# Optimization experiments

Hardware: AMD Instinct MI355X
Metric: run time of the kernel (lower is better)

The kernel has to match this reference:

```python
import jax, jax.numpy as jnp
import numpy as np

B, C, H, W = 8, 384, 32, 32
HEADS, DIM_HEAD = 6, 64
INNER = HEADS * DIM_HEAD  # 384


def setup_inputs() -> dict:
    key = jax.random.key(0)
    ks = jax.random.split(key, 6)
    s = 0.02
    return {
        "query": jax.random.normal(ks[0], (B, C, H, W), jnp.float32),
        "context": jax.random.normal(ks[1], (B, C, H, W), jnp.float32),
        "Wq": jax.random.normal(ks[2], (INNER, C), jnp.float32) * s,
        "Wk": jax.random.normal(ks[3], (INNER, C), jnp.float32) * s,
        "Wv": jax.random.normal(ks[4], (INNER, C), jnp.float32) * s,
        "Wo": jax.random.normal(ks[5], (C, INNER), jnp.float32) * s,
        "bo": jnp.zeros((C,), jnp.float32),
    }


def reference(query, context, Wq, Wk, Wv, Wo, bo):
    scale = DIM_HEAD ** (-0.5)
    b, _, h, w = query.shape
    n = h * w  # tokens
    # 1x1 convs == channel-wise linear projections
    q = jnp.einsum('bchw,oc->bohw', query, Wq)
    k = jnp.einsum('bchw,oc->bohw', context, Wk)
    v = jnp.einsum('bchw,oc->bohw', context, Wv)
    # split heads: [B, heads, dim_head, N]
    q = q.reshape(b, HEADS, DIM_HEAD, n)
    k = k.reshape(b, HEADS, DIM_HEAD, n)
    v = v.reshape(b, HEADS, DIM_HEAD, n)
    # attn[b,h,i,j] = sum_d q[b,h,d,i] k[b,h,d,j] * scale
    attn = jax.nn.softmax(jnp.einsum('bhdn,bhdm->bhnm', q, k) * scale, axis=-1)
    # out[b,h,i,d] = sum_j attn[b,h,i,j] v[b,h,d,j]
    out = jnp.einsum('bhnm,bhdm->bhdn', attn, v)  # [B, heads, dim_head, N]
    out = out.reshape(b, INNER, h, w)
    out = jnp.einsum('bchw,oc->bohw', out, Wo) + bo[None, :, None, None]
    attn_map = attn.mean(axis=(1, 2)).reshape(b, h, w)
    return out, attn_map
```

## Files before the change

kernel.cpp:

```cpp
#include <hip/hip_runtime.h>

#define BATCH 8
#define CCH   384
#define NTOK  1024
#define HEADS 6
#define DHEAD 64
#define QSCALE 0.18033688011112042f

typedef __bf16 bf16x8 __attribute__((ext_vector_type(8)));
typedef float  f32x4  __attribute__((ext_vector_type(4)));

#define MFMA16(a, b, c) __builtin_amdgcn_mfma_f32_16x16x32_bf16((a), (b), (c), 0, 0, 0)

__device__ __forceinline__ short f2b(float x) {
    unsigned u = __float_as_uint(x);
    u += 0x7fffu + ((u >> 16) & 1u);
    return (short)(u >> 16);
}

__device__ __forceinline__ void gld_lds16(const short* gp, short* lp) {
    __builtin_amdgcn_global_load_lds(
        (const __attribute__((address_space(1))) void*)gp,
        (__attribute__((address_space(3))) void*)lp, 16, 0, 0);
}

__device__ __forceinline__ void stage_tile(const short* gbase, size_t gstride,
                                           short* lbase, int wv, int lane) {
#pragma unroll
    for (int t = 0; t < 2; ++t) {
        const int row = t * 8 + (lane >> 3);
        const int c   = (lane & 7) ^ (row & 7);
        gld_lds16(gbase + (size_t)(wv * 16 + row) * gstride + c * 8,
                  lbase + (wv * 16 + t * 8) * 64);
    }
}
__device__ __forceinline__ bf16x8 frag_read(const short* lbase, int row, int c) {
    const int pc = c ^ (row & 7);
    return *(const bf16x8*)(lbase + row * 64 + pc * 8);
}

__device__ __forceinline__ void gemm128_core(
    const short* __restrict__ Ag, const short* __restrict__ Bg,
    short* Ast, short* Bst, f32x4 acc[4][4])
{
    const int tid = threadIdx.x, lane = tid & 63;
    const int l15 = tid & 15, quad = (tid >> 4) & 3, wv = tid >> 6;

    stage_tile(Ag, CCH, Ast, wv, lane);
    stage_tile(Ag + 64 * CCH, CCH, Ast + 4096, wv, lane);
    stage_tile(Bg, CCH, Bst, wv, lane);
    stage_tile(Bg + 64 * CCH, CCH, Bst + 4096, wv, lane);
    __syncthreads();

#pragma unroll
    for (int kc = 0; kc < 6; ++kc) {
        const int cur = kc & 1;
        if (kc < 5) {
            short* An = Ast + (cur ^ 1) * 8192;
            short* Bn = Bst + (cur ^ 1) * 8192;
            stage_tile(Ag + (kc + 1) * 64, CCH, An, wv, lane);
            stage_tile(Ag + (kc + 1) * 64 + 64 * CCH, CCH, An + 4096, wv, lane);
            stage_tile(Bg + (kc + 1) * 64, CCH, Bn, wv, lane);
            stage_tile(Bg + (kc + 1) * 64 + 64 * CCH, CCH, Bn + 4096, wv, lane);
        }
        const short* Atile = Ast + cur * 8192 + (wv >> 1) * 4096;
        const short* Btile = Bst + cur * 8192 + (wv & 1) * 4096;
#pragma unroll
        for (int h = 0; h < 2; ++h) {
            bf16x8 a[4], b[4];
#pragma unroll
            for (int s = 0; s < 4; ++s) {
                a[s] = frag_read(Atile, s * 16 + l15, h * 4 + quad);
                b[s] = frag_read(Btile, s * 16 + l15, h * 4 + quad);
            }
#pragma unroll
            for (int si = 0; si < 4; ++si)
#pragma unroll
                for (int sj = 0; sj < 4; ++sj)
                    acc[si][sj] = MFMA16(a[si], b[sj], acc[si][sj]);
        }
        __syncthreads();
    }
}

__device__ __forceinline__ void epilogue_bf16(
    f32x4 acc[4][4], short* cbuf,
    short* __restrict__ out, size_t obase, int ostride)
{
    const int tid = threadIdx.x;
    const int l15 = tid & 15, quad = (tid >> 4) & 3, wv = tid >> 6;
    const int wi = (wv >> 1) * 64, wj = (wv & 1) * 64;
    __syncthreads();
#pragma unroll
    for (int si = 0; si < 4; ++si)
#pragma unroll
        for (int sj = 0; sj < 4; ++sj)
#pragma unroll
            for (int rr = 0; rr < 4; ++rr)
                cbuf[(wi + si * 16 + quad * 4 + rr) * 128 + wj + sj * 16 + l15] =
                    f2b(acc[si][sj][rr]);
    __syncthreads();
#pragma unroll
    for (int pass = 0; pass < 8; ++pass) {
        const int row = pass * 16 + (tid >> 4);
        bf16x8 vchunk = *(const bf16x8*)(cbuf + row * 128 + l15 * 8);
        *(bf16x8*)(out + obase + (size_t)row * ostride + l15 * 8) = vchunk;
    }
}

__global__ __launch_bounds__(256) void prep(
    const float* __restrict__ Xq, const float* __restrict__ Xc,
    const float* __restrict__ w0, const float* __restrict__ w1,
    const float* __restrict__ w2, const float* __restrict__ w3,
    short* __restrict__ Xtq, short* __restrict__ Xtc,
    short* __restrict__ o0, short* __restrict__ o1,
    short* __restrict__ o2, short* __restrict__ o3,
    float* __restrict__ amap)
{
    __shared__ float tile[64][65];
    const int id = blockIdx.x, tid = threadIdx.x;
    if (id < 1536) {
        const int zz = id % 16, t = id / 16;
        const int n0 = (t % 16) * 64, c0 = (t / 16) * 64;
        const float* X = (zz < 8) ? Xq : Xc;
        short* Xt      = (zz < 8) ? Xtq : Xtc;
        const int b = zz & 7;
        const int tx = tid & 15, ty = tid >> 4;
#pragma unroll
        for (int rr = 0; rr < 4; ++rr) {
            const int c = rr * 16 + ty;
            float4 v = *(const float4*)&X[((size_t)(b * CCH + c0 + c)) * NTOK + n0 + tx * 4];
            tile[c][tx * 4 + 0] = v.x; tile[c][tx * 4 + 1] = v.y;
            tile[c][tx * 4 + 2] = v.z; tile[c][tx * 4 + 3] = v.w;
        }
        __syncthreads();
        const int n = tid >> 2, cb = (tid & 3) * 16;
        short tmp[16];
#pragma unroll
        for (int cc = 0; cc < 16; ++cc) tmp[cc] = f2b(tile[cb + cc][n]);
        short* dst = &Xt[((size_t)(b * NTOK + n0 + n)) * CCH + c0 + cb];
        *(int4*)dst = *(int4*)&tmp[0];
        *(int4*)(dst + 8) = *(int4*)&tmp[8];
    } else if (id < 2112) {
        const int w = id - 1536;
        const int which = w / 144;
        const int idx = (w % 144) * 256 + tid;
        const float* s = which == 0 ? w0 : which == 1 ? w1 : which == 2 ? w2 : w3;
        short* d       = which == 0 ? o0 : which == 1 ? o1 : which == 2 ? o2 : o3;
        float4 v = ((const float4*)s)[idx];
        short4 o = make_short4(f2b(v.x), f2b(v.y), f2b(v.z), f2b(v.w));
        ((short4*)d)[idx] = o;
    } else {
        const int o = (id - 2112) * 1024 + tid * 4;
        float4 z = {0.f, 0.f, 0.f, 0.f};
        *(float4*)&amap[o] = z;
    }
}

__global__ __launch_bounds__(256, 2) void gemm_qkv(
    const short* __restrict__ xtq, const short* __restrict__ xtc,
    const short* __restrict__ wq, const short* __restrict__ wk,
    const short* __restrict__ wvm,
    short* __restrict__ qout, short* __restrict__ kout, short* __restrict__ vout)
{
    __shared__ __align__(16) short Ast[2][8192];
    __shared__ __align__(16) short Bst[2][8192];
    const int id = blockIdx.x;
    const int b = id & 7, r = id >> 3;
    const int which = r / 24, tt = r % 24;

    const short *Ag, *Bg;
    short* out;
    size_t obase;
    int ostride;
    if (which < 2) {
        const int it = tt / 3, jt = tt % 3;
        const short* x = (which == 0) ? xtq : xtc;
        const short* W = (which == 0) ? wq : wk;
        Ag = x + ((size_t)(b * NTOK + it * 128)) * CCH;
        Bg = W + (size_t)(jt * 128) * CCH;
        out = (which == 0) ? qout : kout;
        obase = ((size_t)(b * NTOK + it * 128)) * CCH + jt * 128;
        ostride = CCH;
    } else {
        const int ct = tt % 3, nt = tt / 3;
        Ag = wvm + (size_t)(ct * 128) * CCH;
        Bg = xtc + ((size_t)(b * NTOK + nt * 128)) * CCH;
        out = vout;
        obase = ((size_t)(b * CCH + ct * 128)) * NTOK + nt * 128;
        ostride = NTOK;
    }

    f32x4 z4 = {0.f, 0.f, 0.f, 0.f};
    f32x4 acc[4][4];
#pragma unroll
    for (int si = 0; si < 4; ++si)
#pragma unroll
        for (int sj = 0; sj < 4; ++sj) acc[si][sj] = z4;

    gemm128_core(Ag, Bg, &Ast[0][0], &Bst[0][0], acc);

    if (which == 0) {
#pragma unroll
        for (int si = 0; si < 4; ++si)
#pragma unroll
            for (int sj = 0; sj < 4; ++sj)
#pragma unroll
                for (int rr = 0; rr < 4; ++rr)
                    acc[si][sj][rr] *= QSCALE;
    }
    epilogue_bf16(acc, &Ast[0][0], out, obase, ostride);
}

__global__ __launch_bounds__(256, 2) void o_proj(
    const short* __restrict__ wo, const short* __restrict__ omid,
    const float* __restrict__ bias, float* __restrict__ Y)
{
    __shared__ __align__(16) short Ast[2][8192];
    __shared__ __align__(16) short Bst[2][8192];
    const int id = blockIdx.x;
    const int b = id & 7, r = id >> 3;
    const int ct = r % 3, nt = r / 3;

    const short* Ag = wo + (size_t)(ct * 128) * CCH;
    const short* Bg = omid + ((size_t)(b * NTOK + nt * 128)) * CCH;

    f32x4 z4 = {0.f, 0.f, 0.f, 0.f};
    f32x4 acc[4][4];
#pragma unroll
    for (int si = 0; si < 4; ++si)
#pragma unroll
        for (int sj = 0; sj < 4; ++sj) acc[si][sj] = z4;

    gemm128_core(Ag, Bg, &Ast[0][0], &Bst[0][0], acc);

    const int tid = threadIdx.x;
    const int l15 = tid & 15, quad = (tid >> 4) & 3, wv = tid >> 6;
    const int wi = (wv >> 1) * 64, wj = (wv & 1) * 64;
#pragma unroll
    for (int si = 0; si < 4; ++si) {
#pragma unroll
        for (int rr = 0; rr < 4; ++rr) {
            const int ch = ct * 128 + wi + si * 16 + quad * 4 + rr;
            const float bv = bias[ch];
#pragma unroll
            for (int sj = 0; sj < 4; ++sj)
                Y[((size_t)(b * CCH + ch)) * NTOK + nt * 128 + wj + sj * 16 + l15] =
                    acc[si][sj][rr] + bv;
        }
    }
}

__global__ __launch_bounds__(256) void attn(
    const short* __restrict__ qt, const short* __restrict__ kt,
    const short* __restrict__ vc, short* __restrict__ omid,
    float* __restrict__ amap)
{
    __shared__ __align__(16) short Kst[2][64 * 64];
    __shared__ __align__(16) short Vst[2][64 * 64];
    __shared__ __align__(16) short Pst[4][16][64];
    __shared__ float colbuf[2][4][64];

    const int tid = threadIdx.x, lane = tid & 63;
    const int l15 = tid & 15, quad = (tid >> 4) & 3, wv = tid >> 6;
    const int id = blockIdx.x;
    const int b = id & 7, rr_ = id >> 3;
    const int h = rr_ % 6, i0 = (rr_ / 6) * 64;

    const size_t hoff = (size_t)b * NTOK * CCH + h * DHEAD;
    const short* Kg = kt + hoff;
    const short* Vg = vc + ((size_t)(b * CCH + h * DHEAD)) * NTOK;

    const short* qp = qt + hoff + (size_t)(i0 + wv * 16 + l15) * CCH + quad * 8;
    const bf16x8 qa0 = *(const bf16x8*)qp;
    const bf16x8 qa1 = *(const bf16x8*)(qp + 32);

    stage_tile(Kg, CCH, Kst[0], wv, lane);
    __syncthreads();

    float den[4] = {0.f, 0.f, 0.f, 0.f};
    for (int jt = 0; jt < 16; ++jt) {
        const int cur = jt & 1;
        if (jt < 15)
            stage_tile(Kg + (size_t)(jt + 1) * 64 * CCH, CCH, Kst[cur ^ 1], wv, lane);
        f32x4 z4 = {0.f, 0.f, 0.f, 0.f};
        f32x4 s[4] = {z4, z4, z4, z4};
#pragma unroll
        for (int ns = 0; ns < 4; ++ns) {
            const int row = ns * 16 + l15;
            bf16x8 k0 = frag_read(Kst[cur], row, quad);
            bf16x8 k1 = frag_read(Kst[cur], row, quad + 4);
            s[ns] = MFMA16(qa0, k0, s[ns]);
            s[ns] = MFMA16(qa1, k1, s[ns]);
        }
#pragma unroll
        for (int ns = 0; ns < 4; ++ns)
#pragma unroll
            for (int r = 0; r < 4; ++r)
                den[r] += exp2f(s[ns][r]);
        __syncthreads();
    }
#pragma unroll
    for (int r = 0; r < 4; ++r) {
        den[r] += __shfl_xor(den[r], 1);
        den[r] += __shfl_xor(den[r], 2);
        den[r] += __shfl_xor(den[r], 4);
        den[r] += __shfl_xor(den[r], 8);
    }
    float rden[4];
#pragma unroll
    for (int r = 0; r < 4; ++r) rden[r] = 1.0f / den[r];

    stage_tile(Kg, CCH, Kst[0], wv, lane);
    stage_tile(Vg, NTOK, Vst[0], wv, lane);
    __syncthreads();

    f32x4 z4o = {0.f, 0.f, 0.f, 0.f};
    f32x4 oacc[4] = {z4o, z4o, z4o, z4o};
    for (int jt = 0; jt < 16; ++jt) {
        const int cur = jt & 1;
        if (jt < 15) {
            stage_tile(Kg + (size_t)(jt + 1) * 64 * CCH, CCH, Kst[cur ^ 1], wv, lane);
            stage_tile(Vg + (size_t)(jt + 1) * 64, NTOK, Vst[cur ^ 1], wv, lane);
        }
        f32x4 s[4] = {z4o, z4o, z4o, z4o};
#pragma unroll
        for (int ns = 0; ns < 4; ++ns) {
            const int row = ns * 16 + l15;
            bf16x8 k0 = frag_read(Kst[cur], row, quad);
            bf16x8 k1 = frag_read(Kst[cur], row, quad + 4);
            s[ns] = MFMA16(qa0, k0, s[ns]);
            s[ns] = MFMA16(qa1, k1, s[ns]);
        }
        float p[4][4];
#pragma unroll
        for (int ns = 0; ns < 4; ++ns)
#pragma unroll
            for (int r = 0; r < 4; ++r)
                p[ns][r] = exp2f(s[ns][r]) * rden[r];

#pragma unroll
        for (int ns = 0; ns < 4; ++ns) {
            float cs = p[ns][0] + p[ns][1] + p[ns][2] + p[ns][3];
            cs += __shfl_xor(cs, 16);
            cs += __shfl_xor(cs, 32);
            if (quad == 0) colbuf[cur][wv][ns * 16 + l15] = cs;
        }

#pragma unroll
        for (int ns = 0; ns < 4; ++ns) {
            const int c = ns * 2 + (l15 >> 3);
#pragma unroll
            for (int r = 0; r < 4; ++r) {
                const int row = quad * 4 + r;
                Pst[wv][row][((c ^ (row & 7)) << 3) | (l15 & 7)] = f2b(p[ns][r]);
            }
        }
        asm volatile("" ::: "memory");
        const int pc0 = quad ^ (l15 & 7);
        const int pc1 = (quad + 4) ^ (l15 & 7);
        bf16x8 pa0 = *(const bf16x8*)&Pst[wv][l15][pc0 * 8];
        bf16x8 pa1 = *(const bf16x8*)&Pst[wv][l15][pc1 * 8];
        asm volatile("" ::: "memory");

#pragma unroll
        for (int ds = 0; ds < 4; ++ds) {
            const int row = ds * 16 + l15;
            bf16x8 v0 = frag_read(Vst[cur], row, quad);
            bf16x8 v1 = frag_read(Vst[cur], row, quad + 4);
            oacc[ds] = MFMA16(pa0, v0, oacc[ds]);
            oacc[ds] = MFMA16(pa1, v1, oacc[ds]);
        }
        __syncthreads();
        if (tid < 64) {
            const float t = colbuf[cur][0][tid] + colbuf[cur][1][tid]
                          + colbuf[cur][2][tid] + colbuf[cur][3][tid];
            atomicAdd(amap + (size_t)b * NTOK + jt * 64 + tid,
                      t * (1.0f / (HEADS * NTOK)));
        }
    }

#pragma unroll
    for (int ds = 0; ds < 4; ++ds)
#pragma unroll
        for (int r = 0; r < 4; ++r) {
            const int i = i0 + wv * 16 + quad * 4 + r;
            omid[((size_t)(b * NTOK + i)) * CCH + h * DHEAD + ds * 16 + l15] =
                f2b(oacc[ds][r]);
        }
}

extern "C" void kernel_launch(void* const* d_in, const int* in_sizes, int n_in,
                              void* d_out, int out_size, void* d_ws, size_t ws_size,
                              hipStream_t stream)
{
    const float* query   = (const float*)d_in[0];
    const float* context = (const float*)d_in[1];
    const float* Wq      = (const float*)d_in[2];
    const float* Wk      = (const float*)d_in[3];
    const float* Wv      = (const float*)d_in[4];
    const float* Wo      = (const float*)d_in[5];
    const float* bo      = (const float*)d_in[6];

    float* out = (float*)d_out;
    const size_t out_elems = (size_t)BATCH * CCH * NTOK;
    float* attn_map = out + out_elems;

    short* ws = (short*)d_ws;
    const size_t XT = (size_t)BATCH * NTOK * CCH;
    const size_t WSZ = (size_t)CCH * CCH;
    short* xtq  = ws;
    short* xtc  = xtq + XT;
    short* wqb  = xtc + XT;
    short* wkb  = wqb + WSZ;
    short* wvb  = wkb + WSZ;
    short* wob  = wvb + WSZ;
    short* qtb  = wob + WSZ;
    short* ktb  = qtb + XT;
    short* vcb  = ktb + XT;
    short* omid = vcb + XT;

    const dim3 blk(256);

    prep<<<dim3(2120), blk, 0, stream>>>(query, context, Wq, Wk, Wv, Wo,
                                         xtq, xtc, wqb, wkb, wvb, wob, attn_map);

    gemm_qkv<<<dim3(576), blk, 0, stream>>>(xtq, xtc, wqb, wkb, wvb,
                                            qtb, ktb, vcb);

    attn<<<dim3(768), blk, 0, stream>>>(qtb, ktb, vcb, omid, attn_map);

    o_proj<<<dim3(192), blk, 0, stream>>>(wob, omid, bo, out);
}
```

Baseline: 167.3 us.

## Fuse four kernels into persistent megakernel with software grid barriers

Measured after the change: 449.8 us. +168.9%, slower.

```diff
diff --git a/kernel.cpp b/kernel.cpp
--- a/kernel.cpp
+++ b/kernel.cpp
@@ -7,6 +7,8 @@
 #define DHEAD 64
 #define QSCALE 0.18033688011112042f
 
+#define NBLK 512
+
 typedef __bf16 bf16x8 __attribute__((ext_vector_type(8)));
 typedef float  f32x4  __attribute__((ext_vector_type(4)));
 
@@ -39,32 +41,34 @@
     return *(const bf16x8*)(lbase + row * 64 + pc * 8);
 }
 
-__device__ __forceinline__ void gemm128_core(
+__device__ __forceinline__ void gbar(int* cnt) {
+    __syncthreads();
+    if (threadIdx.x == 0) {
+        __threadfence();
+        __hip_atomic_fetch_add(cnt, 1, __ATOMIC_RELEASE, __HIP_MEMORY_SCOPE_AGENT);
+        while (__hip_atomic_load(cnt, __ATOMIC_ACQUIRE, __HIP_MEMORY_SCOPE_AGENT) < NBLK)
+            __builtin_amdgcn_s_sleep(2);
+        __threadfence();
+    }
+    __syncthreads();
+}
+
+__device__ __forceinline__ void gemm128_core_sb(
     const short* __restrict__ Ag, const short* __restrict__ Bg,
     short* Ast, short* Bst, f32x4 acc[4][4])
 {
     const int tid = threadIdx.x, lane = tid & 63;
     const int l15 = tid & 15, quad = (tid >> 4) & 3, wv = tid >> 6;
 
-    stage_tile(Ag, CCH, Ast, wv, lane);
-    stage_tile(Ag + 64 * CCH, CCH, Ast + 4096, wv, lane);
-    stage_tile(Bg, CCH, Bst, wv, lane);
-    stage_tile(Bg + 64 * CCH, CCH, Bst + 4096, wv, lane);
-    __syncthreads();
-
 #pragma unroll
     for (int kc = 0; kc < 6; ++kc) {
-        const int cur = kc & 1;
-        if (kc < 5) {
-            short* An = Ast + (cur ^ 1) * 8192;
-            short* Bn = Bst + (cur ^ 1) * 8192;
-            stage_tile(Ag + (kc + 1) * 64, CCH, An, wv, lane);
-            stage_tile(Ag + (kc + 1) * 64 + 64 * CCH, CCH, An + 4096, wv, lane);
-            stage_tile(Bg + (kc + 1) * 64, CCH, Bn, wv, lane);
-            stage_tile(Bg + (kc + 1) * 64 + 64 * CCH, CCH, Bn + 4096, wv, lane);
-        }
-        const short* Atile = Ast + cur * 8192 + (wv >> 1) * 4096;
-        const short* Btile = Bst + cur * 8192 + (wv & 1) * 4096;
+        stage_tile(Ag + kc * 64, CCH, Ast, wv, lane);
+        stage_tile(Ag + kc * 64 + 64 * CCH, CCH, Ast + 4096, wv, lane);
+        stage_tile(Bg + kc * 64, CCH, Bst, wv, lane);
+        stage_tile(Bg + kc * 64 + 64 * CCH, CCH, Bst + 4096, wv, lane);
+        __syncthreads();
+        const short* Atile = Ast + (wv >> 1) * 4096;
+        const short* Btile = Bst + (wv & 1) * 4096;
 #pragma unroll
         for (int h = 0; h < 2; ++h) {
             bf16x8 a[4], b[4];
@@ -108,18 +112,16 @@
     }
 }
 
-__global__ __launch_bounds__(256) void prep(
-    const float* __restrict__ Xq, const float* __restrict__ Xc,
-    const float* __restrict__ w0, const float* __restrict__ w1,
-    const float* __restrict__ w2, const float* __restrict__ w3,
-    short* __restrict__ Xtq, short* __restrict__ Xtc,
-    short* __restrict__ o0, short* __restrict__ o1,
-    short* __restrict__ o2, short* __restrict__ o3,
-    float* __restrict__ amap)
-{
-    __shared__ float tile[64][65];
-    const int id = blockIdx.x, tid = threadIdx.x;
+__device__ __forceinline__ void prep_unit(
+    int id, char* smem,
+    const float* Xq, const float* Xc,
+    const float* w0, const float* w1, const float* w2, const float* w3,
+    short* Xtq, short* Xtc,
+    short* o0, short* o1, short* o2, short* o3, float* amap)
+{
+    const int tid = threadIdx.x;
     if (id < 1536) {
+        float (*tile)[65] = (float(*)[65])smem;
         const int zz = id % 16, t = id / 16;
         const int n0 = (t % 16) * 64, c0 = (t / 16) * 64;
         const float* X = (zz < 8) ? Xq : Xc;
@@ -157,15 +159,14 @@
     }
 }
 
-__global__ __launch_bounds__(256, 2) void gemm_qkv(
-    const short* __restrict__ xtq, const short* __restrict__ xtc,
-    const short* __restrict__ wq, const short* __restrict__ wk,
-    const short* __restrict__ wvm,
-    short* __restrict__ qout, short* __restrict__ kout, short* __restrict__ vout)
-{
-    __shared__ __align__(16) short Ast[2][8192];
-    __shared__ __align__(16) short Bst[2][8192];
-    const int id = blockIdx.x;
+__device__ __forceinline__ void gemm_qkv_unit(
+    int id, char* smem,
+    const short* xtq, const short* xtc,
+    const short* wq, const short* wk, const short* wvm,
+    short* qout, short* kout, short* vout)
+{
+    short* Ast = (short*)smem;
+    short* Bst = (short*)(smem + 16384);
     const int b = id & 7, r = id >> 3;
     const int which = r / 24, tt = r % 24;
 
@@ -198,7 +199,7 @@
 #pragma unroll
         for (int sj = 0; sj < 4; ++sj) acc[si][sj] = z4;
 
-    gemm128_core(Ag, Bg, &Ast[0][0], &Bst[0][0], acc);
+    gemm128_core_sb(Ag, Bg, Ast, Bst, acc);
 
     if (which == 0) {
 #pragma unroll
@@ -209,16 +210,15 @@
                 for (int rr = 0; rr < 4; ++rr)
                     acc[si][sj][rr] *= QSCALE;
     }
-    epilogue_bf16(acc, &Ast[0][0], out, obase, ostride);
-}
-
-__global__ __launch_bounds__(256, 2) void o_proj(
-    const short* __restrict__ wo, const short* __restrict__ omid,
-    const float* __restrict__ bias, float* __restrict__ Y)
-{
-    __shared__ __align__(16) short Ast[2][8192];
-    __shared__ __align__(16) short Bst[2][8192];
-    const int id = blockIdx.x;
+    epilogue_bf16(acc, (short*)smem, out, obase, ostride);
+}
+
+__device__ __forceinline__ void o_proj_unit(
+    int id, char* smem,
+    const short* wo, const short* omid, const float* bias, float* Y)
+{
+    short* Ast = (short*)smem;
+    short* Bst = (short*)(smem + 16384);
     const int b = id & 7, r = id >> 3;
     const int ct = r % 3, nt = r / 3;
 
@@ -232,7 +232,7 @@
 #pragma unroll
         for (int sj = 0; sj < 4; ++sj) acc[si][sj] = z4;
 
-    gemm128_core(Ag, Bg, &Ast[0][0], &Bst[0][0], acc);
+    gemm128_core_sb(Ag, Bg, Ast, Bst, acc);
 
     const int tid = threadIdx.x;
     const int l15 = tid & 15, quad = (tid >> 4) & 3, wv = tid >> 6;
@@ -251,19 +251,18 @@
     }
 }
 
-__global__ __launch_bounds__(256) void attn(
-    const short* __restrict__ qt, const short* __restrict__ kt,
-    const short* __restrict__ vc, short* __restrict__ omid,
-    float* __restrict__ amap)
-{
-    __shared__ __align__(16) short Kst[2][64 * 64];
-    __shared__ __align__(16) short Vst[2][64 * 64];
-    __shared__ __align__(16) short Pst[4][16][64];
-    __shared__ float colbuf[2][4][64];
+__device__ __forceinline__ void attn_unit(
+    int id, char* smem,
+    const short* qt, const short* kt, const short* vc,
+    short* omid, float* amap)
+{
+    short* Kst    = (short*)smem;
+    short* Vst    = (short*)(smem + 16384);
+    short* Pst    = (short*)(smem + 32768);
+    float* colbuf = (float*)(smem + 40960);
 
     const int tid = threadIdx.x, lane = tid & 63;
     const int l15 = tid & 15, quad = (tid >> 4) & 3, wv = tid >> 6;
-    const int id = blockIdx.x;
     const int b = id & 7, rr_ = id >> 3;
     const int h = rr_ % 6, i0 = (rr_ / 6) * 64;
 
@@ -275,21 +274,22 @@
     const bf16x8 qa0 = *(const bf16x8*)qp;
     const bf16x8 qa1 = *(const bf16x8*)(qp + 32);
 
-    stage_tile(Kg, CCH, Kst[0], wv, lane);
+    stage_tile(Kg, CCH, Kst, wv, lane);
     __syncthreads();
 
     float den[4] = {0.f, 0.f, 0.f, 0.f};
     for (int jt = 0; jt < 16; ++jt) {
         const int cur = jt & 1;
         if (jt < 15)
-            stage_tile(Kg + (size_t)(jt + 1) * 64 * CCH, CCH, Kst[cur ^ 1], wv, lane);
+            stage_tile(Kg + (size_t)(jt + 1) * 64 * CCH, CCH,
+                       Kst + (cur ^ 1) * 4096, wv, lane);
         f32x4 z4 = {0.f, 0.f, 0.f, 0.f};
         f32x4 s[4] = {z4, z4, z4, z4};
 #pragma unroll
         for (int ns = 0; ns < 4; ++ns) {
             const int row = ns * 16 + l15;
-            bf16x8 k0 = frag_read(Kst[cur], row, quad);
-            bf16x8 k1 = frag_read(Kst[cur], row, quad + 4);
+            bf16x8 k0 = frag_read(Kst + cur * 4096, row, quad);
+            bf16x8 k1 = frag_read(Kst + cur * 4096, row, quad + 4);
             s[ns] = MFMA16(qa0, k0, s[ns]);
             s[ns] = MFMA16(qa1, k1, s[ns]);
         }
@@ -311,8 +311,8 @@
 #pragma unroll
     for (int r = 0; r < 4; ++r) rden[r] = 1.0f / den[r];
 
-    stage_tile(Kg, CCH, Kst[0], wv, lane);
-    stage_tile(Vg, NTOK, Vst[0], wv, lane);
+    stage_tile(Kg, CCH, Kst, wv, lane);
+    stage_tile(Vg, NTOK, Vst, wv, lane);
     __syncthreads();
 
     f32x4 z4o = {0.f, 0.f, 0.f, 0.f};
@@ -320,15 +320,17 @@
     for (int jt = 0; jt < 16; ++jt) {
         const int cur = jt & 1;
         if (jt < 15) {
-            stage_tile(Kg + (size_t)(jt + 1) * 64 * CCH, CCH, Kst[cur ^ 1], wv, lane);
-            stage_tile(Vg + (size_t)(jt + 1) * 64, NTOK, Vst[cur ^ 1], wv, lane);
+            stage_tile(Kg + (size_t)(jt + 1) * 64 * CCH, CCH,
+                       Kst + (cur ^ 1) * 4096, wv, lane);
+            stage_tile(Vg + (size_t)(jt + 1) * 64, NTOK,
+                       Vst + (cur ^ 1) * 4096, wv, lane);
         }
         f32x4 s[4] = {z4o, z4o, z4o, z4o};
 #pragma unroll
         for (int ns = 0; ns < 4; ++ns) {
             const int row = ns * 16 + l15;
-            bf16x8 k0 = frag_read(Kst[cur], row, quad);
-            bf16x8 k1 = frag_read(Kst[cur], row, quad + 4);
+            bf16x8 k0 = frag_read(Kst + cur * 4096, row, quad);
+            bf16x8 k1 = frag_read(Kst + cur * 4096, row, quad + 4);
             s[ns] = MFMA16(qa0, k0, s[ns]);
             s[ns] = MFMA16(qa1, k1, s[ns]);
         }
@@ -344,7 +346,7 @@
             float cs = p[ns][0] + p[ns][1] + p[ns][2] + p[ns][3];
             cs += __shfl_xor(cs, 16);
             cs += __shfl_xor(cs, 32);
-            if (quad == 0) colbuf[cur][wv][ns * 16 + l15] = cs;
+            if (quad == 0) colbuf[cur * 256 + wv * 64 + ns * 16 + l15] = cs;
         }
 
 #pragma unroll
@@ -353,28 +355,31 @@
 #pragma unroll
             for (int r = 0; r < 4; ++r) {
                 const int row = quad * 4 + r;
-                Pst[wv][row][((c ^ (row & 7)) << 3) | (l15 & 7)] = f2b(p[ns][r]);
+                Pst[wv * 1024 + row * 64 + (((c ^ (row & 7)) << 3) | (l15 & 7))] =
+                    f2b(p[ns][r]);
             }
         }
         asm volatile("" ::: "memory");
         const int pc0 = quad ^ (l15 & 7);
         const int pc1 = (quad + 4) ^ (l15 & 7);
-        bf16x8 pa0 = *(const bf16x8*)&Pst[wv][l15][pc0 * 8];
-        bf16x8 pa1 = *(const bf16x8*)&Pst[wv][l15][pc1 * 8];
+        bf16x8 pa0 = *(const bf16x8*)&Pst[wv * 1024 + l15 * 64 + pc0 * 8];
+        bf16x8 pa1 = *(const bf16x8*)&Pst[wv * 1024 + l15 * 64 + pc1 * 8];
         asm volatile("" ::: "memory");
 
 #pragma unroll
         for (int ds = 0; ds < 4; ++ds) {
             const int row = ds * 16 + l15;
-            bf16x8 v0 = frag_read(Vst[cur], row, quad);
-            bf16x8 v1 = frag_read(Vst[cur], row, quad + 4);
+            bf16x8 v0 = frag_read(Vst + cur * 4096, row, quad);
+            bf16x8 v1 = frag_read(Vst + cur * 4096, row, quad + 4);
             oacc[ds] = MFMA16(pa0, v0, oacc[ds]);
             oacc[ds] = MFMA16(pa1, v1, oacc[ds]);
         }
         __syncthreads();
         if (tid < 64) {
-            const float t = colbuf[cur][0][tid] + colbuf[cur][1][tid]
-                          + colbuf[cur][2][tid] + colbuf[cur][3][tid];
+            const float t = colbuf[cur * 256 + 0 * 64 + tid]
+                          + colbuf[cur * 256 + 1 * 64 + tid]
+                          + colbuf[cur * 256 + 2 * 64 + tid]
+                          + colbuf[cur * 256 + 3 * 64 + tid];
             atomicAdd(amap + (size_t)b * NTOK + jt * 64 + tid,
                       t * (1.0f / (HEADS * NTOK)));
         }
@@ -388,6 +393,42 @@
             omid[((size_t)(b * NTOK + i)) * CCH + h * DHEAD + ds * 16 + l15] =
                 f2b(oacc[ds][r]);
         }
+}
+
+__global__ __launch_bounds__(256, 2) void mega(
+    const float* __restrict__ Xq, const float* __restrict__ Xc,
+    const float* __restrict__ w0, const float* __restrict__ w1,
+    const float* __restrict__ w2, const float* __restrict__ w3,
+    const float* __restrict__ bo,
+    short* xtq, short* xtc,
+    short* wqb, short* wkb, short* wvb, short* wob,
+    short* qtb, short* ktb, short* vcb, short* omid,
+    float* out, float* amap, int* bar)
+{
+    __shared__ __align__(16) char smem[43008];
+    const int bid = blockIdx.x;
+
+    for (int u = bid; u < 2120; u += NBLK) {
+        prep_unit(u, smem, Xq, Xc, w0, w1, w2, w3,
+                  xtq, xtc, wqb, wkb, wvb, wob, amap);
+        __syncthreads();
+    }
+    gbar(&bar[0]);
+
+    for (int u = bid; u < 576; u += NBLK) {
+        gemm_qkv_unit(u, smem, xtq, xtc, wqb, wkb, wvb, qtb, ktb, vcb);
+        __syncthreads();
+    }
+    gbar(&bar[1]);
+
+    for (int u = bid; u < 768; u += NBLK) {
+        attn_unit(u, smem, qtb, ktb, vcb, omid, amap);
+        __syncthreads();
+    }
+    gbar(&bar[2]);
+
+    if (bid < 192)
+        o_proj_unit(bid, smem, wob, omid, bo, out);
 }
 
 extern "C" void kernel_launch(void* const* d_in, const int* in_sizes, int n_in,
@@ -419,16 +460,12 @@
     short* ktb  = qtb + XT;
     short* vcb  = ktb + XT;
     short* omid = vcb + XT;
-
-    const dim3 blk(256);
-
-    prep<<<dim3(2120), blk, 0, stream>>>(query, context, Wq, Wk, Wv, Wo,
-                                         xtq, xtc, wqb, wkb, wvb, wob, attn_map);
-
-    gemm_qkv<<<dim3(576), blk, 0, stream>>>(xtq, xtc, wqb, wkb, wvb,
-                                            qtb, ktb, vcb);
-
-    attn<<<dim3(768), blk, 0, stream>>>(qtb, ktb, vcb, omid, attn_map);
-
-    o_proj<<<dim3(192), blk, 0, stream>>>(wob, omid, bo, out);
-}
+    int*   bar  = (int*)(omid + XT);
+
+    hipMemsetAsync(bar, 0, 4 * sizeof(int), stream);
+
+    mega<<<dim3(NBLK), dim3(256), 0, stream>>>(
+        query, context, Wq, Wk, Wv, Wo, bo,
+        xtq, xtc, wqb, wkb, wvb, wob,
+        qtb, ktb, vcb, omid, out, attn_map, bar);
+}
```

## Double attention query tile per block to share K/V staging across eight waves

Applied to the files above, without the earlier changes.

New measurement: 169.3 us. No clear change (+1.2%).

```diff
diff --git a/kernel.cpp b/kernel.cpp
--- a/kernel.cpp
+++ b/kernel.cpp
@@ -33,6 +33,13 @@
         gld_lds16(gbase + (size_t)(wv * 16 + row) * gstride + c * 8,
                   lbase + (wv * 16 + t * 8) * 64);
     }
+}
+__device__ __forceinline__ void stage_tile8(const short* gbase, size_t gstride,
+                                            short* lbase, int wv, int lane) {
+    const int row = wv * 8 + (lane >> 3);
+    const int c   = (lane & 7) ^ (row & 7);
+    gld_lds16(gbase + (size_t)row * gstride + c * 8,
+              lbase + (wv * 8) * 64);
 }
 __device__ __forceinline__ bf16x8 frag_read(const short* lbase, int row, int c) {
     const int pc = c ^ (row & 7);
@@ -251,21 +258,21 @@
     }
 }
 
-__global__ __launch_bounds__(256) void attn(
+__global__ __launch_bounds__(512) void attn(
     const short* __restrict__ qt, const short* __restrict__ kt,
     const short* __restrict__ vc, short* __restrict__ omid,
     float* __restrict__ amap)
 {
     __shared__ __align__(16) short Kst[2][64 * 64];
     __shared__ __align__(16) short Vst[2][64 * 64];
-    __shared__ __align__(16) short Pst[4][16][64];
-    __shared__ float colbuf[2][4][64];
+    __shared__ __align__(16) short Pst[8][16][64];
+    __shared__ float colbuf[2][8][64];
 
     const int tid = threadIdx.x, lane = tid & 63;
     const int l15 = tid & 15, quad = (tid >> 4) & 3, wv = tid >> 6;
     const int id = blockIdx.x;
     const int b = id & 7, rr_ = id >> 3;
-    const int h = rr_ % 6, i0 = (rr_ / 6) * 64;
+    const int h = rr_ % 6, i0 = (rr_ / 6) * 128;
 
     const size_t hoff = (size_t)b * NTOK * CCH + h * DHEAD;
     const short* Kg = kt + hoff;
@@ -275,14 +282,14 @@
     const bf16x8 qa0 = *(const bf16x8*)qp;
     const bf16x8 qa1 = *(const bf16x8*)(qp + 32);
 
-    stage_tile(Kg, CCH, Kst[0], wv, lane);
+    stage_tile8(Kg, CCH, Kst[0], wv, lane);
     __syncthreads();
 
     float den[4] = {0.f, 0.f, 0.f, 0.f};
     for (int jt = 0; jt < 16; ++jt) {
         const int cur = jt & 1;
         if (jt < 15)
-            stage_tile(Kg + (size_t)(jt + 1) * 64 * CCH, CCH, Kst[cur ^ 1], wv, lane);
+            stage_tile8(Kg + (size_t)(jt + 1) * 64 * CCH, CCH, Kst[cur ^ 1], wv, lane);
         f32x4 z4 = {0.f, 0.f, 0.f, 0.f};
         f32x4 s[4] = {z4, z4, z4, z4};
 #pragma unroll
@@ -311,8 +318,8 @@
 #pragma unroll
     for (int r = 0; r < 4; ++r) rden[r] = 1.0f / den[r];
 
-    stage_tile(Kg, CCH, Kst[0], wv, lane);
-    stage_tile(Vg, NTOK, Vst[0], wv, lane);
+    stage_tile8(Kg, CCH, Kst[0], wv, lane);
+    stage_tile8(Vg, NTOK, Vst[0], wv, lane);
     __syncthreads();
 
     f32x4 z4o = {0.f, 0.f, 0.f, 0.f};
@@ -320,8 +327,8 @@
     for (int jt = 0; jt < 16; ++jt) {
         const int cur = jt & 1;
         if (jt < 15) {
-            stage_tile(Kg + (size_t)(jt + 1) * 64 * CCH, CCH, Kst[cur ^ 1], wv, lane);
-            stage_tile(Vg + (size_t)(jt + 1) * 64, NTOK, Vst[cur ^ 1], wv, lane);
+            stage_tile8(Kg + (size_t)(jt + 1) * 64 * CCH, CCH, Kst[cur ^ 1], wv, lane);
+            stage_tile8(Vg + (size_t)(jt + 1) * 64, NTOK, Vst[cur ^ 1], wv, lane);
         }
         f32x4 s[4] = {z4o, z4o, z4o, z4o};
 #pragma unroll
@@ -373,8 +380,9 @@
         }
         __syncthreads();
         if (tid < 64) {
-            const float t = colbuf[cur][0][tid] + colbuf[cur][1][tid]
-                          + colbuf[cur][2][tid] + colbuf[cur][3][tid];
+            float t = 0.f;
+#pragma unroll
+            for (int w = 0; w < 8; ++w) t += colbuf[cur][w][tid];
             atomicAdd(amap + (size_t)b * NTOK + jt * 64 + tid,
                       t * (1.0f / (HEADS * NTOK)));
         }
@@ -420,15 +428,14 @@
     short* vcb  = ktb + XT;
     short* omid = vcb + XT;
 
-    const dim3 blk(256);
-
-    prep<<<dim3(2120), blk, 0, stream>>>(query, context, Wq, Wk, Wv, Wo,
-                                         xtq, xtc, wqb, wkb, wvb, wob, attn_map);
-
-    gemm_qkv<<<dim3(576), blk, 0, stream>>>(xtq, xtc, wqb, wkb, wvb,
-                                            qtb, ktb, vcb);
-
-    attn<<<dim3(768), blk, 0, stream>>>(qtb, ktb, vcb, omid, attn_map);
-
-    o_proj<<<dim3(192), blk, 0, stream>>>(wob, omid, bo, out);
-}
+    prep<<<dim3(2120), dim3(256), 0, stream>>>(query, context, Wq, Wk, Wv, Wo,
+                                               xtq, xtc, wqb, wkb, wvb, wob,
+                                               attn_map);
+
+    gemm_qkv<<<dim3(576), dim3(256), 0, stream>>>(xtq, xtc, wqb, wkb, wvb,
+                                                  qtb, ktb, vcb);
+
+    attn<<<dim3(384), dim3(512), 0, stream>>>(qtb, ktb, vcb, omid, attn_map);
+
+    o_proj<<<dim3(192), dim3(256), 0, stream>>>(wob, omid, bo, out);
+}
```
